# Kernel optimization log

Hardware: AMD Instinct MI355X
Metric: run time of the kernel (lower is better)

## Reference

```python
import jax, jax.numpy as jnp
import numpy as np
import math

B, S, D, H, M, R = 4, 1024, 1024, 16, 4, 64
DH = D // H
EPS = 1e-8

def setup_inputs() -> dict:
    key = jax.random.key(0)
    ks = jax.random.split(key, 8)
    sc = 0.02
    return {
        'x': jax.random.normal(ks[0], (B, S, D), jnp.float32),
        'Wk': jax.random.normal(ks[1], (D, D), jnp.float32) * sc,
        'bk': jnp.zeros((D,), jnp.float32),
        'Wq': jax.random.normal(ks[2], (D, D), jnp.float32) * sc,
        'bq': jnp.zeros((D,), jnp.float32),
        'Wv': jax.random.normal(ks[3], (D, D), jnp.float32) * sc,
        'bv': jnp.zeros((D,), jnp.float32),
        'mask1': jax.random.normal(ks[4], (M, R, S), jnp.float32) * sc,
        'mask2': jax.random.normal(ks[5], (M, R, S), jnp.float32) * sc,
        'roll_back': jax.random.randint(ks[6], (M, S, S), 0, S, jnp.int64),
    }

def reference(x, Wk, bk, Wq, bq, Wv, bv, mask1, mask2, roll_back):
    def proj(W, b):
        # torch Linear: x @ W^T + b ; reshape to [B, H, S, DH]
        y = jnp.dot(x, W.T) + b
        return y.reshape(B, S, H, DH).transpose(0, 2, 1, 3)
    k = proj(Wk, bk)
    q = proj(Wq, bq)
    v = proj(Wv, bv)
    # learnable low-rank mask: [M, S, S]
    learnable_mask = jnp.einsum('mrs,mrt->mst', mask1, mask2)
    # gather along last dim with roll_back indices
    gathered = jnp.take_along_axis(learnable_mask, roll_back, axis=-1)  # [M, S, S]
    att = jnp.einsum('bhsd,bhtd->bhst', q, k) / math.sqrt(DH)  # [B, H, S, S]
    att = att.reshape(B, H // M, M, S, S) * gathered[None, None]
    att = att.reshape(B, H, S, S)
    # Frobenius norm over last two dims per (B, H)
    fro = jnp.sqrt(jnp.sum(att * att, axis=(-2, -1), keepdims=True))
    att = att / (fro + EPS)
    out = jnp.einsum('bhst,bhtd->bhsd', att, v)
    return out.transpose(0, 2, 1, 3).reshape(B, S, D)
```

## Files before the change

kernel.cpp:

```cpp
#include <hip/hip_runtime.h>
#include <hip/hip_bf16.h>
#include <stdint.h>

typedef __attribute__((ext_vector_type(8))) __bf16 bf16x8;
typedef __attribute__((ext_vector_type(4))) float  f32x4;
typedef __attribute__((ext_vector_type(16))) float f32x16;

__device__ __forceinline__ ushort f2bf(float f) {
    union { float f; uint32_t u; } v; v.f = f;
    uint32_t u = v.u;
    uint32_t r = 0x7FFFu + ((u >> 16) & 1u);
    return (ushort)((u + r) >> 16);
}
__device__ __forceinline__ float bf2f(ushort u) {
    union { uint32_t u; float f; } v; v.u = ((uint32_t)u) << 16;
    return v.f;
}
__device__ __forceinline__ unsigned cvtpk(float lo, float hi) {
    unsigned r;
    asm("v_cvt_pk_bf16_f32 %0, %1, %2" : "=v"(r) : "v"(lo), "v"(hi));
    return r;
}

typedef __attribute__((address_space(3))) uint32_t lds_u32_t;
typedef const __attribute__((address_space(1))) uint32_t glb_u32_t;
__device__ __forceinline__ void async_copy16(const void* g, void* l) {
    __builtin_amdgcn_global_load_lds((glb_u32_t*)g, (lds_u32_t*)l, 16, 0, 0);
}

__global__ __launch_bounds__(256) void prework(
    const float* __restrict__ x, const float* __restrict__ wk,
    const float* __restrict__ wq, const float* __restrict__ wv,
    ushort* __restrict__ xb, ushort* __restrict__ wball,
    const float* __restrict__ m1, const float* __restrict__ m2,
    const int* __restrict__ rb, ushort* __restrict__ gth,
    float* __restrict__ ssb)
{
    __shared__ float As8[64 * 8];
    __shared__ float lmS[8 * 1024];
    const int tid = threadIdx.x;

    if (blockIdx.x < 512) {
        const int s0 = (blockIdx.x & 127) * 8;
        const int m = blockIdx.x >> 7;

        if (tid < 128) {
            int r = tid >> 1, half = tid & 1;
            *(float4*)&As8[r * 8 + half * 4] =
                *(const float4*)&m1[(m * 64 + r) * 1024 + s0 + half * 4];
        }
        __syncthreads();

        f32x4 acc8[8];
        #pragma unroll
        for (int s = 0; s < 8; s++) acc8[s] = (f32x4){0.f, 0.f, 0.f, 0.f};
        const float* m2b = m2 + m * 65536 + tid * 4;
        #pragma unroll 4
        for (int r = 0; r < 64; r++) {
            float4 b4 = *(const float4*)&m2b[r * 1024];
            f32x4 b = (f32x4){b4.x, b4.y, b4.z, b4.w};
            #pragma unroll
            for (int s = 0; s < 8; s++) {
                float a = As8[r * 8 + s];
                acc8[s] += a * b;
            }
        }
        #pragma unroll
        for (int s = 0; s < 8; s++)
            *(f32x4*)&lmS[s * 1024 + tid * 4] = acc8[s];
        __syncthreads();

        const int base = (m * 1024 + s0) * 1024;
        #pragma unroll
        for (int i = 0; i < 8; i++) {
            int c = tid + i * 256;
            int row = c >> 8, j = (c & 255) * 4;
            int4 idx = *(const int4*)&rb[base + row * 1024 + j];
            ushort4 o;
            o.x = f2bf(lmS[row * 1024 + (idx.x & 1023)] * 0.125f);
            o.y = f2bf(lmS[row * 1024 + (idx.y & 1023)] * 0.125f);
            o.z = f2bf(lmS[row * 1024 + (idx.z & 1023)] * 0.125f);
            o.w = f2bf(lmS[row * 1024 + (idx.w & 1023)] * 0.125f);
            *(ushort4*)&gth[base + row * 1024 + j] = o;
        }
    } else if (blockIdx.x < 7680) {
        int i = (blockIdx.x - 512) * 256 + tid;
        const float* src; ushort* dst; int j;
        if (i < 1048576) { src = x; dst = xb; j = i; }
        else {
            int t = i - 1048576;
            int z = t >> 18;
            j = t & 262143;
            src = (z == 0) ? wk : (z == 1) ? wq : wv;
            dst = wball + z * 1048576;
        }
        float4 f = ((const float4*)src)[j];
        ushort4 o;
        o.x = f2bf(f.x); o.y = f2bf(f.y); o.z = f2bf(f.z); o.w = f2bf(f.w);
        ((ushort4*)dst)[j] = o;
    } else {
        if (tid < 64) ssb[tid] = 0.f;
    }
}

__global__ __launch_bounds__(256) void proj_gemm(
    const ushort* __restrict__ xb, const ushort* __restrict__ wball,
    const float* __restrict__ bk, const float* __restrict__ bq, const float* __restrict__ bv,
    ushort* __restrict__ kd, ushort* __restrict__ qd, ushort* __restrict__ vd)
{
    __shared__ ushort As[3 * 128 * 32];
    __shared__ ushort Bs[3 * 128 * 32];
    const int z = blockIdx.z;
    const int row0 = blockIdx.x * 128;
    const int col0 = blockIdx.y * 128;
    const ushort* wb = wball + z * 1048576;
    const int tid = threadIdx.x;
    const int lane = tid & 63, wave = tid >> 6;
    const int quad = lane >> 4, m15 = lane & 15;
    const int wr = wave >> 1, wc = wave & 1;

    f32x4 acc[4][4];
    for (int i = 0; i < 4; i++)
        for (int j = 0; j < 4; j++) acc[i][j] = (f32x4){0.f, 0.f, 0.f, 0.f};

#define STAGE(BI, KK) do {                                                        \
        _Pragma("unroll")                                                         \
        for (int i_ = 0; i_ < 2; i_++) {                                          \
            int c_ = tid + i_ * 256;                                  \
            int r_ = c_ >> 2, cjp_ = c_ & 3;                                      \
            int cj_ = cjp_ ^ ((r_ >> 1) & 3);                                     \
            async_copy16(&xb[(row0 + r_) * 1024 + (KK) + cj_ * 8],                \
                         &As[(BI) * 4096 + c_ * 8]);                              \
            async_copy16(&wb[(col0 + r_) * 1024 + (KK) + cj_ * 8],                \
                         &Bs[(BI) * 4096 + c_ * 8]);                              \
        }                                                                         \
    } while (0)

#define COMPUTE(BI) do {                                                          \
        const ushort* a_ = &As[(BI) * 4096];                                      \
        const ushort* b_ = &Bs[(BI) * 4096];                                      \
        bf16x8 af[4], bfv[4];                                                     \
        _Pragma("unroll")                                                         \
        for (int fr = 0; fr < 4; fr++) {                                          \
            int row = wr * 64 + fr * 16 + m15;                                    \
            af[fr] = *(const bf16x8*)&a_[row * 32 + ((quad ^ ((row >> 1) & 3)) * 8)]; \
        }                                                                         \
        _Pragma("unroll")                                                         \
        for (int fc = 0; fc < 4; fc++) {                                          \
            int row = wc * 64 + fc * 16 + m15;                                    \
            bfv[fc] = *(const bf16x8*)&b_[row * 32 + ((quad ^ ((row >> 1) & 3)) * 8)]; \
        }                                                                         \
        _Pragma("unroll")                                                         \
        for (int fr = 0; fr < 4; fr++)                                            \
            _Pragma("unroll")                                                     \
            for (int fc = 0; fc < 4; fc++)                                        \
                acc[fr][fc] = __builtin_amdgcn_mfma_f32_16x16x32_bf16(            \
                    af[fr], bfv[fc], acc[fr][fc], 0, 0, 0);                       \
    } while (0)

    STAGE(0, 0);
    STAGE(1, 32);

    int cur = 0;
    #pragma unroll 3
    for (int t = 0; t < 30; ++t) {
        int sb = cur + 2; if (sb >= 3) sb -= 3;
        STAGE(sb, (t + 2) * 32);
        asm volatile("s_waitcnt vmcnt(8)" ::: "memory");
        __builtin_amdgcn_s_barrier();
        COMPUTE(cur);
        __builtin_amdgcn_s_barrier();
        cur = (cur == 2) ? 0 : cur + 1;
    }
    asm volatile("s_waitcnt vmcnt(4)" ::: "memory");
    __builtin_amdgcn_s_barrier();
    COMPUTE(cur);
    cur = (cur == 2) ? 0 : cur + 1;
    asm volatile("s_waitcnt vmcnt(0)" ::: "memory");
    __builtin_amdgcn_s_barrier();
    COMPUTE(cur);

#undef STAGE
#undef COMPUTE

    const float* bias = (z == 0) ? bk : (z == 1) ? bq : bv;
    ushort* dstA = (z == 0) ? kd : qd;
    for (int fr = 0; fr < 4; fr++) {
        int ibase = row0 + wr * 64 + fr * 16 + quad * 4;
        int b_ = ibase >> 10, s = ibase & 1023;
        for (int fc = 0; fc < 4; fc++) {
            int j = col0 + wc * 64 + fc * 16 + m15;
            int h = j >> 6, dh = j & 63;
            float bb = bias[j];
            if (z < 2) {
                for (int r = 0; r < 4; r++)
                    dstA[((b_ * 16 + h) * 1024 + (s + r)) * 64 + dh] = f2bf(acc[fr][fc][r] + bb);
            } else {
                ushort4 o;
                o.x = f2bf(acc[fr][fc][0] + bb);
                o.y = f2bf(acc[fr][fc][1] + bb);
                o.z = f2bf(acc[fr][fc][2] + bb);
                o.w = f2bf(acc[fr][fc][3] + bb);
                *(ushort4*)&vd[((b_ * 16 + h) * 64 + dh) * 1024 + s] = o;
            }
        }
    }
}

__global__ __launch_bounds__(256, 4) void attention(
    const ushort* __restrict__ qd, const ushort* __restrict__ kd, const ushort* __restrict__ vd,
    const ushort* __restrict__ gth, float* __restrict__ O, float* __restrict__ ss)
{
    __shared__ __align__(16) char ldsraw[28176];
    ushort* Ks  = (ushort*)ldsraw;
    ushort* Vs  = (ushort*)(ldsraw + 9216);
    ushort* Ms  = (ushort*)(ldsraw + 18432);
    float*  red = (float*)(ldsraw + 28160);
    float*  fbuf = (float*)ldsraw;

    const int s0 = blockIdx.x * 64;
    const int bh = blockIdx.y;
    const int mm = bh & 3;
    const int tid = threadIdx.x, lane = tid & 63, wave = tid >> 6;
    const int l31 = lane & 31, hl = lane >> 5;
    const int wr2 = wave >> 1, wc2 = wave & 1;

    const int r0_ = tid >> 3,          o0_ = (tid & 7) * 8;
    const int r1_ = (tid + 256) >> 3,  o1_ = ((tid + 256) & 7) * 8;

    const ushort* kdb = kd + bh * 65536;
    const ushort* vdb = vd + bh * 65536;
    const ushort* gbase = gth + mm * 1048576 + s0 * 1024;

    const int srow = wr2 * 32 + l31;
    const int tb   = wc2 * 32 + 4 * hl;

    *(uint4*)&Ks[r0_ * 72 + o0_] = *(const uint4*)&qd[(bh * 1024 + s0 + r0_) * 64 + o0_];
    *(uint4*)&Ks[r1_ * 72 + o1_] = *(const uint4*)&qd[(bh * 1024 + s0 + r1_) * 64 + o1_];
    uint4 kr0 = *(const uint4*)&kdb[r0_ * 64 + o0_];
    uint4 kr1 = *(const uint4*)&kdb[r1_ * 64 + o1_];
    uint4 vr0 = *(const uint4*)&vdb[r0_ * 1024 + o0_];
    uint4 vr1 = *(const uint4*)&vdb[r1_ * 1024 + o1_];
    uint4 mr0 = *(const uint4*)&gbase[r0_ * 1024 + o0_];
    uint4 mr1 = *(const uint4*)&gbase[r1_ * 1024 + o1_];
    __syncthreads();
    bf16x8 qf[4];
    #pragma unroll
    for (int kk = 0; kk < 4; kk++)
        qf[kk] = *(const bf16x8*)&Ks[srow * 72 + kk * 16 + hl * 8];
    __syncthreads();

    *(uint4*)&Ks[r0_ * 72 + o0_] = kr0;
    *(uint4*)&Ks[r1_ * 72 + o1_] = kr1;
    *(uint4*)&Vs[r0_ * 72 + o0_] = vr0;
    *(uint4*)&Vs[r1_ * 72 + o1_] = vr1;
    *(uint2*)&Ms[r0_ * 76 + o0_]     = make_uint2(mr0.x, mr0.y);
    *(uint2*)&Ms[r0_ * 76 + o0_ + 4] = make_uint2(mr0.z, mr0.w);
    *(uint2*)&Ms[r1_ * 76 + o1_]     = make_uint2(mr1.x, mr1.y);
    *(uint2*)&Ms[r1_ * 76 + o1_ + 4] = make_uint2(mr1.z, mr1.w);
    kr0 = *(const uint4*)&kdb[(64 + r0_) * 64 + o0_];
    kr1 = *(const uint4*)&kdb[(64 + r1_) * 64 + o1_];
    vr0 = *(const uint4*)&vdb[r0_ * 1024 + 64 + o0_];
    vr1 = *(const uint4*)&vdb[r1_ * 1024 + 64 + o1_];
    mr0 = *(const uint4*)&gbase[r0_ * 1024 + 64 + o0_];
    mr1 = *(const uint4*)&gbase[r1_ * 1024 + 64 + o1_];
    __syncthreads();

    f32x16 oaccA, oaccB;
    #pragma unroll
    for (int i = 0; i < 16; i++) { oaccA[i] = 0.f; oaccB[i] = 0.f; }
    float ss0 = 0.f, ss1 = 0.f, ss2 = 0.f, ss3 = 0.f;

    for (int t = 0; t < 16; ++t) {
        f32x16 p;
        #pragma unroll
        for (int i = 0; i < 16; i++) p[i] = 0.f;
        __builtin_amdgcn_s_setprio(1);
        #pragma unroll
        for (int kk = 0; kk < 4; kk++) {
            bf16x8 kf = *(const bf16x8*)&Ks[(wc2 * 32 + l31) * 72 + kk * 16 + hl * 8];
            p = __builtin_amdgcn_mfma_f32_32x32x16_bf16(kf, qf[kk], p, 0, 0, 0);
        }
        __builtin_amdgcn_s_setprio(0);
        unsigned u[8];
        #pragma unroll
        for (int g = 0; g < 4; g++) {
            ushort4 mk = *(const ushort4*)&Ms[srow * 76 + tb + 8 * g];
            float pv0 = p[4 * g + 0] * bf2f(mk.x);
            float pv1 = p[4 * g + 1] * bf2f(mk.y);
            float pv2 = p[4 * g + 2] * bf2f(mk.z);
            float pv3 = p[4 * g + 3] * bf2f(mk.w);
            ss0 += pv0 * pv0; ss1 += pv1 * pv1;
            ss2 += pv2 * pv2; ss3 += pv3 * pv3;
            u[2 * g]     = cvtpk(pv0, pv1);
            u[2 * g + 1] = cvtpk(pv2, pv3);
        }
        auto r02 = __builtin_amdgcn_permlane32_swap(u[0], u[2], false, false);
        auto r13 = __builtin_amdgcn_permlane32_swap(u[1], u[3], false, false);
        auto r46 = __builtin_amdgcn_permlane32_swap(u[4], u[6], false, false);
        auto r57 = __builtin_amdgcn_permlane32_swap(u[5], u[7], false, false);
        union { unsigned q[4]; bf16x8 v; } af0, af1;
        af0.q[0] = r02[0]; af0.q[1] = r13[0]; af0.q[2] = r02[1]; af0.q[3] = r13[1];
        af1.q[0] = r46[0]; af1.q[1] = r57[0]; af1.q[2] = r46[1]; af1.q[3] = r57[1];
        __builtin_amdgcn_s_setprio(1);
        {
            const ushort* vrA = &Vs[l31 * 72 + wc2 * 32];
            bf16x8 b00 = *(const bf16x8*)&vrA[hl * 8];
            bf16x8 b01 = *(const bf16x8*)&vrA[16 + hl * 8];
            oaccA = __builtin_amdgcn_mfma_f32_32x32x16_bf16(af0.v, b00, oaccA, 0, 0, 0);
            oaccA = __builtin_amdgcn_mfma_f32_32x32x16_bf16(af1.v, b01, oaccA, 0, 0, 0);
            const ushort* vrB = &Vs[(32 + l31) * 72 + wc2 * 32];
            bf16x8 b10 = *(const bf16x8*)&vrB[hl * 8];
            bf16x8 b11 = *(const bf16x8*)&vrB[16 + hl * 8];
            oaccB = __builtin_amdgcn_mfma_f32_32x32x16_bf16(af0.v, b10, oaccB, 0, 0, 0);
            oaccB = __builtin_amdgcn_mfma_f32_32x32x16_bf16(af1.v, b11, oaccB, 0, 0, 0);
        }
        __builtin_amdgcn_s_setprio(0);
        __syncthreads();
        if (t < 15) {
            *(uint4*)&Ks[r0_ * 72 + o0_] = kr0;
            *(uint4*)&Ks[r1_ * 72 + o1_] = kr1;
            *(uint4*)&Vs[r0_ * 72 + o0_] = vr0;
            *(uint4*)&Vs[r1_ * 72 + o1_] = vr1;
            *(uint2*)&Ms[r0_ * 76 + o0_]     = make_uint2(mr0.x, mr0.y);
            *(uint2*)&Ms[r0_ * 76 + o0_ + 4] = make_uint2(mr0.z, mr0.w);
            *(uint2*)&Ms[r1_ * 76 + o1_]     = make_uint2(mr1.x, mr1.y);
            *(uint2*)&Ms[r1_ * 76 + o1_ + 4] = make_uint2(mr1.z, mr1.w);
            if (t < 14) {
                const int tn = (t + 2) * 64;
                kr0 = *(const uint4*)&kdb[(tn + r0_) * 64 + o0_];
                kr1 = *(const uint4*)&kdb[(tn + r1_) * 64 + o1_];
                vr0 = *(const uint4*)&vdb[r0_ * 1024 + tn + o0_];
                vr1 = *(const uint4*)&vdb[r1_ * 1024 + tn + o1_];
                mr0 = *(const uint4*)&gbase[r0_ * 1024 + tn + o0_];
                mr1 = *(const uint4*)&gbase[r1_ * 1024 + tn + o1_];
            }
            __syncthreads();
        }
    }

    if (wc2 == 1) {
        #pragma unroll
        for (int reg = 0; reg < 16; reg++) {
            int row = wr2 * 32 + (reg & 3) + 8 * (reg >> 2) + 4 * hl;
            fbuf[row * 66 + l31]      = oaccA[reg];
            fbuf[row * 66 + 32 + l31] = oaccB[reg];
        }
    }
    __syncthreads();
    if (wc2 == 0) {
        #pragma unroll
        for (int reg = 0; reg < 16; reg++) {
            int rl = (reg & 3) + 8 * (reg >> 2) + 4 * hl;
            int s = s0 + wr2 * 32 + rl;
            float a = oaccA[reg] + fbuf[(wr2 * 32 + rl) * 66 + l31];
            float b = oaccB[reg] + fbuf[(wr2 * 32 + rl) * 66 + 32 + l31];
            O[(bh * 1024 + s) * 64 + l31]      = a;
            O[(bh * 1024 + s) * 64 + 32 + l31] = b;
        }
    }
    float ssacc = (ss0 + ss1) + (ss2 + ss3);
    for (int off = 32; off; off >>= 1) ssacc += __shfl_down(ssacc, off, 64);
    if (lane == 0) red[wave] = ssacc;
    __syncthreads();
    if (tid == 0) atomicAdd(&ss[bh], red[0] + red[1] + red[2] + red[3]);
}

__global__ __launch_bounds__(256) void normalize_out(const float* __restrict__ O,
                                                     const float* __restrict__ ss,
                                                     float* __restrict__ out)
{
    int gid = blockIdx.x * 256 + threadIdx.x;
    int e = gid * 4;
    int bh = e >> 16;
    float inv = 1.f / (sqrtf(ss[bh]) + 1e-8f);
    float4 v4 = *(const float4*)&O[e];
    int b_ = bh >> 4, h = bh & 15;
    int s = (e >> 6) & 1023, dh = e & 63;
    float4 o4 = {v4.x * inv, v4.y * inv, v4.z * inv, v4.w * inv};
    *(float4*)&out[((b_ * 1024 + s) * 16 + h) * 64 + dh] = o4;
}

extern "C" void kernel_launch(void* const* d_in, const int* in_sizes, int n_in,
                              void* d_out, int out_size, void* d_ws, size_t ws_size,
                              hipStream_t stream) {
    const float* x  = (const float*)d_in[0];
    const float* Wk = (const float*)d_in[1];
    const float* bk = (const float*)d_in[2];
    const float* Wq = (const float*)d_in[3];
    const float* bq = (const float*)d_in[4];
    const float* Wv = (const float*)d_in[5];
    const float* bv = (const float*)d_in[6];
    const float* m1 = (const float*)d_in[7];
    const float* m2 = (const float*)d_in[8];
    const int*   rb = (const int*)d_in[9];
    float* out = (float*)d_out;

    char* ws = (char*)d_ws;
    ushort* xb    = (ushort*)(ws);
    ushort* wball = (ushort*)(ws + 8388608);
    ushort* kd    = (ushort*)(ws + 14680064);
    ushort* qd    = (ushort*)(ws + 23068672);
    ushort* vd    = (ushort*)(ws + 31457280);
    float*  O     = (float*)(ws + 39845888);
    ushort* gth   = (ushort*)(ws + 56623104);
    float*  ssb   = (float*)(ws + 65011712);

    prework<<<7681, 256, 0, stream>>>(x, Wk, Wq, Wv, xb, wball, m1, m2, rb, gth, ssb);
    proj_gemm<<<dim3(32, 8, 3), 256, 0, stream>>>(xb, wball, bk, bq, bv, kd, qd, vd);
    attention<<<dim3(16, 64), 256, 0, stream>>>(qd, kd, vd, gth, O, ssb);
    normalize_out<<<4096, 256, 0, stream>>>(O, ssb, out);
}
```

Baseline: 178.5 us.

## Fuse Frobenius normalization into attention via per-head grid counter spin-wait

Removes the separate normalize_out kernel and the fp32 O intermediate. Each attention block adds its partial sum of squares and bumps a per-(b,h) counter, then spins until all 16 blocks of that head have arrived. It then scales its accumulators and writes the final output directly. This saves a full write and read of a 16 MB buffer and one launch. The price is an inter-block dependency that relies on all 16 blocks of a head being co-resident, and it can deadlock or stall if they are not.

```diff
diff --git a/kernel.cpp b/kernel.cpp
--- a/kernel.cpp
+++ b/kernel.cpp
@@ -34,7 +34,7 @@
     ushort* __restrict__ xb, ushort* __restrict__ wball,
     const float* __restrict__ m1, const float* __restrict__ m2,
     const int* __restrict__ rb, ushort* __restrict__ gth,
-    float* __restrict__ ssb)
+    float* __restrict__ ssb, int* __restrict__ cnt)
 {
     __shared__ float As8[64 * 8];
     __shared__ float lmS[8 * 1024];
@@ -99,7 +99,7 @@
         o.x = f2bf(f.x); o.y = f2bf(f.y); o.z = f2bf(f.z); o.w = f2bf(f.w);
         ((ushort4*)dst)[j] = o;
     } else {
-        if (tid < 64) ssb[tid] = 0.f;
+        if (tid < 64) { ssb[tid] = 0.f; cnt[tid] = 0; }
     }
 }
 
@@ -209,7 +209,8 @@
 
 __global__ __launch_bounds__(256, 4) void attention(
     const ushort* __restrict__ qd, const ushort* __restrict__ kd, const ushort* __restrict__ vd,
-    const ushort* __restrict__ gth, float* __restrict__ O, float* __restrict__ ss)
+    const ushort* __restrict__ gth, float* __restrict__ out,
+    float* __restrict__ ss, int* __restrict__ cnt)
 {
     __shared__ __align__(16) char ldsraw[28176];
     ushort* Ks  = (ushort*)ldsraw;
@@ -339,6 +340,9 @@
         }
     }
 
+    float ssacc = (ss0 + ss1) + (ss2 + ss3);
+    for (int off = 32; off; off >>= 1) ssacc += __shfl_down(ssacc, off, 64);
+    if (lane == 0) red[wave] = ssacc;
     if (wc2 == 1) {
         #pragma unroll
         for (int reg = 0; reg < 16; reg++) {
@@ -348,37 +352,38 @@
         }
     }
     __syncthreads();
+    if (tid == 0) {
+        atomicAdd(&ss[bh], red[0] + red[1] + red[2] + red[3]);
+        __hip_atomic_fetch_add(&cnt[bh], 1, __ATOMIC_RELEASE, __HIP_MEMORY_SCOPE_AGENT);
+    }
     if (wc2 == 0) {
+        #pragma unroll
+        for (int reg = 0; reg < 16; reg++) {
+            int rl = (reg & 3) + 8 * (reg >> 2) + 4 * hl;
+            oaccA[reg] += fbuf[(wr2 * 32 + rl) * 66 + l31];
+            oaccB[reg] += fbuf[(wr2 * 32 + rl) * 66 + 32 + l31];
+        }
+    }
+
+    if (tid == 0) {
+        while (__hip_atomic_load(&cnt[bh], __ATOMIC_ACQUIRE,
+                                 __HIP_MEMORY_SCOPE_AGENT) < 16) {}
+    }
+    __syncthreads();
+
+    float sst = __hip_atomic_load(&ss[bh], __ATOMIC_RELAXED, __HIP_MEMORY_SCOPE_AGENT);
+    float inv = 1.f / (sqrtf(sst) + 1e-8f);
+    if (wc2 == 0) {
+        const int b_ = bh >> 4, h = bh & 15;
         #pragma unroll
         for (int reg = 0; reg < 16; reg++) {
             int rl = (reg & 3) + 8 * (reg >> 2) + 4 * hl;
             int s = s0 + wr2 * 32 + rl;
-            float a = oaccA[reg] + fbuf[(wr2 * 32 + rl) * 66 + l31];
-            float b = oaccB[reg] + fbuf[(wr2 * 32 + rl) * 66 + 32 + l31];
-            O[(bh * 1024 + s) * 64 + l31]      = a;
-            O[(bh * 1024 + s) * 64 + 32 + l31] = b;
-        }
-    }
-    float ssacc = (ss0 + ss1) + (ss2 + ss3);
-    for (int off = 32; off; off >>= 1) ssacc += __shfl_down(ssacc, off, 64);
-    if (lane == 0) red[wave] = ssacc;
-    __syncthreads();
-    if (tid == 0) atomicAdd(&ss[bh], red[0] + red[1] + red[2] + red[3]);
-}
-
-__global__ __launch_bounds__(256) void normalize_out(const float* __restrict__ O,
-                                                     const float* __restrict__ ss,
-                                                     float* __restrict__ out)
-{
-    int gid = blockIdx.x * 256 + threadIdx.x;
-    int e = gid * 4;
-    int bh = e >> 16;
-    float inv = 1.f / (sqrtf(ss[bh]) + 1e-8f);
-    float4 v4 = *(const float4*)&O[e];
-    int b_ = bh >> 4, h = bh & 15;
-    int s = (e >> 6) & 1023, dh = e & 63;
-    float4 o4 = {v4.x * inv, v4.y * inv, v4.z * inv, v4.w * inv};
-    *(float4*)&out[((b_ * 1024 + s) * 16 + h) * 64 + dh] = o4;
+            float* op = &out[((b_ * 1024 + s) * 16 + h) * 64];
+            op[l31]      = oaccA[reg] * inv;
+            op[32 + l31] = oaccB[reg] * inv;
+        }
+    }
 }
 
 extern "C" void kernel_launch(void* const* d_in, const int* in_sizes, int n_in,
@@ -402,12 +407,12 @@
     ushort* kd    = (ushort*)(ws + 14680064);
     ushort* qd    = (ushort*)(ws + 23068672);
     ushort* vd    = (ushort*)(ws + 31457280);
-    float*  O     = (float*)(ws + 39845888);
+    int*    cntb  = (int*)(ws + 39845888);
     ushort* gth   = (ushort*)(ws + 56623104);
     float*  ssb   = (float*)(ws + 65011712);
 
-    prework<<<7681, 256, 0, stream>>>(x, Wk, Wq, Wv, xb, wball, m1, m2, rb, gth, ssb);
+    prework<<<7681, 256, 0, stream>>>(x, Wk, Wq, Wv, xb, wball, m1, m2, rb, gth,
+                                      ssb, cntb);
     proj_gemm<<<dim3(32, 8, 3), 256, 0, stream>>>(xb, wball, bk, bq, bv, kd, qd, vd);
-    attention<<<dim3(16, 64), 256, 0, stream>>>(qd, kd, vd, gth, O, ssb);
-    normalize_out<<<4096, 256, 0, stream>>>(O, ssb, out);
-}
+    attention<<<dim3(16, 64), 256, 0, stream>>>(qd, kd, vd, gth, out, ssb, cntb);
+}
```

After: 283.3 us. 1.59x slower.
